# Optimization experiments

Measured on AMD Instinct MI355X. Metric: run time of the kernel, lower is better.

Reference implementation:

```python
import jax, jax.numpy as jnp
import numpy as np

N_HEADS = 12

def setup_inputs() -> dict:
    key = jax.random.key(0)
    ks = jax.random.split(key, 3)
    B, C, T = 4, 768, 2048
    x = jax.random.normal(ks[0], (B, C, T), dtype=jnp.float32)
    mask = jnp.ones((B, 1, 1, T), dtype=jnp.int32)  # all valid; masked_fill where mask==0
    Wqkv = jax.random.normal(ks[1], (3 * C, C), dtype=jnp.float32) * 0.02
    bqkv = jnp.zeros((3 * C,), dtype=jnp.float32)
    Wout = jax.random.normal(ks[2], (C, C), dtype=jnp.float32) * 0.02
    bout = jnp.zeros((C,), dtype=jnp.float32)
    return {"x": x, "mask": mask, "Wqkv": Wqkv, "bqkv": bqkv, "Wout": Wout, "bout": bout}


def reference(x, mask, Wqkv, bqkv, Wout, bout):
    B, C, T = x.shape
    H = N_HEADS
    d = C // H
    scale = 1.0 / jnp.sqrt(jnp.asarray(d, x.dtype))
    # 1x1 Conv1d == per-timestep matmul over channels
    qkv = jnp.einsum('oc,bct->bot', Wqkv, x) + bqkv[None, :, None]  # [B,3C,T]
    # channel dim splits as [3, H, d] per the torch view(B,3,H,d,T)
    qkv = qkv.reshape(B, 3, H, d, T).transpose(0, 1, 2, 4, 3)       # [B,3,H,T,d]
    q, k, v = qkv[:, 0], qkv[:, 1], qkv[:, 2]
    score = jnp.einsum('bhtd,bhsd->bhts', q, k) * scale             # [B,H,T,T]
    score = jnp.where(mask == 0, jnp.asarray(-10000.0, score.dtype), score)
    attn = jax.nn.softmax(score, axis=-1)  # dropout: eval mode (identity)
    o = jnp.einsum('bhts,bhsd->bhtd', attn, v)                      # [B,H,T,d]
    o = o.transpose(0, 1, 3, 2).reshape(B, C, T)                    # [B,C,T]
    return jnp.einsum('oc,bct->bot', Wout, o) + bout[None, :, None]
```

## Files before the change

### kernel.cpp

```cpp
#include <hip/hip_runtime.h>
#include <hip/hip_bf16.h>
#include <stdint.h>

#define B_   4
#define C_   768
#define T_   2048
#define H_   12
#define D_   64
#define O3_  2304

typedef __attribute__((ext_vector_type(4))) float f32x4;
typedef __attribute__((ext_vector_type(8))) short bf16x8;

__device__ __forceinline__ unsigned short f2bf(float f) {
  union { float f; unsigned int u; } v; v.f = f;
  unsigned int r = v.u + 0x7fffu + ((v.u >> 16) & 1u);
  return (unsigned short)(r >> 16);
}

__device__ __forceinline__ unsigned int pack2bf(float a, float b) {
  __hip_bfloat162 h2 = __float22bfloat162_rn(make_float2(a, b));
  union { __hip_bfloat162 h; unsigned int u; } cv; cv.h = h2;
  return cv.u;
}

__device__ __forceinline__ float fexp2(float x) {
#if __has_builtin(__builtin_amdgcn_exp2f)
  return __builtin_amdgcn_exp2f(x);
#else
  return exp2f(x);
#endif
}

__device__ __forceinline__ void async16(const void* g, void* lds) {
#if __has_builtin(__builtin_amdgcn_global_load_lds)
  __builtin_amdgcn_global_load_lds((const __attribute__((address_space(1))) void*)g,
                                   (__attribute__((address_space(3))) void*)lds, 16, 0, 0);
#else
  int lane = threadIdx.x & 63;
  *((uint4*)((char*)lds + lane * 16)) = *((const uint4*)g);
#endif
}


__global__ void cvt_f32_bf16(const float* __restrict__ in,
                             unsigned short* __restrict__ out, int n4) {
  int i = blockIdx.x * 256 + threadIdx.x;
  if (i < n4) {
    float4 f = ((const float4*)in)[i];
    ushort4 o;
    o.x = f2bf(f.x); o.y = f2bf(f.y); o.z = f2bf(f.z); o.w = f2bf(f.w);
    ((ushort4*)out)[i] = o;
  }
}

__global__ void make_bias(const int* __restrict__ mask, float* __restrict__ mbias, int n) {
  int i = blockIdx.x * 256 + threadIdx.x;
  if (i < n) mbias[i] = (mask[i] == 0) ? -14426.950408f : 0.0f;
}

__global__ void transpose_x(const float* __restrict__ x,
                            unsigned short* __restrict__ xT) {
  __shared__ unsigned short tile[32][33];
  int b = blockIdx.z;
  int c0 = blockIdx.y * 32;
  int t0 = blockIdx.x * 32;
  int tid = threadIdx.x;
  {
    int cl = tid >> 3;
    int tl = (tid & 7) * 4;
    float4 f = *(const float4*)(x + ((size_t)b * C_ + c0 + cl) * T_ + t0 + tl);
    tile[tl + 0][cl] = f2bf(f.x);
    tile[tl + 1][cl] = f2bf(f.y);
    tile[tl + 2][cl] = f2bf(f.z);
    tile[tl + 3][cl] = f2bf(f.w);
  }
  __syncthreads();
  {
    int tl = tid >> 3;
    int cl = (tid & 7) * 4;
    ushort4 o;
    o.x = tile[tl][cl + 0]; o.y = tile[tl][cl + 1];
    o.z = tile[tl][cl + 2]; o.w = tile[tl][cl + 3];
    *(ushort4*)(xT + ((size_t)b * T_ + t0 + tl) * C_ + c0 + cl) = o;
  }
}

__global__ __launch_bounds__(256)
void gemm_qkv(const unsigned short* __restrict__ xT,
              const unsigned short* __restrict__ W1,
              const float* __restrict__ bqkv,
              unsigned short* __restrict__ Qb,
              unsigned short* __restrict__ Kb,
              unsigned short* __restrict__ Vb) {
  __shared__ unsigned short sA[2][128 * 32];
  __shared__ unsigned short sB[2][128 * 32];

  const int b   = blockIdx.z;
  const int o0  = blockIdx.y * 128;
  const int t0  = blockIdx.x * 128;
  const int tid = threadIdx.x;
  const int wave = tid >> 6, lane = tid & 63;
  const int q = lane >> 4, ln = lane & 15;
  const int tw = wave >> 1, ow = wave & 1;

  const unsigned short* Ax = xT + (size_t)b * T_ * C_;
  const int srow = lane >> 2;
  const int scol = (lane & 3) * 8;

  const f32x4 ZERO = {0.f, 0.f, 0.f, 0.f};
  f32x4 acc[4][4];
#pragma unroll
  for (int mi = 0; mi < 4; ++mi)
#pragma unroll
    for (int ni = 0; ni < 4; ++ni) acc[mi][ni] = ZERO;

#pragma unroll
  for (int j = 0; j < 2; ++j) {
    const int chunk = wave * 2 + j;
    const int row = chunk * 16 + srow;
    async16(Ax + (size_t)(t0 + row) * C_ + scol, &sA[0][chunk * 512]);
    async16(W1 + (size_t)(o0 + row) * C_ + scol, &sB[0][chunk * 512]);
  }

  for (int i = 0; i < 24; ++i) {
    const int buf = i & 1;
    __syncthreads();
    if (i < 23) {
      const int k0 = (i + 1) * 32;
#pragma unroll
      for (int j = 0; j < 2; ++j) {
        const int chunk = wave * 2 + j;
        const int row = chunk * 16 + srow;
        async16(Ax + (size_t)(t0 + row) * C_ + k0 + scol, &sA[buf ^ 1][chunk * 512]);
        async16(W1 + (size_t)(o0 + row) * C_ + k0 + scol, &sB[buf ^ 1][chunk * 512]);
      }
    }

    bf16x8 aF[4], bF[4];
#pragma unroll
    for (int mi = 0; mi < 4; ++mi)
      aF[mi] = *(const bf16x8*)(&sA[buf][(tw * 64 + mi * 16 + ln) * 32 + q * 8]);
#pragma unroll
    for (int ni = 0; ni < 4; ++ni)
      bF[ni] = *(const bf16x8*)(&sB[buf][(ow * 64 + ni * 16 + ln) * 32 + q * 8]);
#pragma unroll
    for (int mi = 0; mi < 4; ++mi)
#pragma unroll
      for (int ni = 0; ni < 4; ++ni)
        acc[mi][ni] = __builtin_amdgcn_mfma_f32_16x16x32_bf16(aF[mi], bF[ni], acc[mi][ni], 0, 0, 0);
  }

  const float QSCL = 0.125f * 1.44269504f;
#pragma unroll
  for (int ni = 0; ni < 4; ++ni) {
    const int o = o0 + ow * 64 + ni * 16 + ln;
    const float bias = bqkv[o];
    const int which = o / C_;
    const int rem = o - which * C_;
    const int bh = b * H_ + (rem >> 6);
    const int dd = rem & 63;
#pragma unroll
    for (int mi = 0; mi < 4; ++mi) {
      const int tb = t0 + tw * 64 + mi * 16 + q * 4;
      f32x4 v = acc[mi][ni];
      if (which == 0) {
#pragma unroll
        for (int r = 0; r < 4; ++r)
          Qb[((size_t)bh * T_ + tb + r) * D_ + dd] = f2bf((v[r] + bias) * QSCL);
      } else if (which == 1) {
#pragma unroll
        for (int r = 0; r < 4; ++r) {
          const int s = tb + r;
          const int cp = (dd >> 3) ^ (s & 7);
          Kb[((size_t)bh * T_ + s) * 64 + (cp << 3) + (dd & 7)] = f2bf(v[r] + bias);
        }
      } else {
        const int tile = tb >> 6, si = tb & 63;
        const int cp = (si >> 3) ^ (dd & 7);
        ushort4 pk;
        pk.x = f2bf(v[0] + bias);
        pk.y = f2bf(v[1] + bias);
        pk.z = f2bf(v[2] + bias);
        pk.w = f2bf(v[3] + bias);
        *(ushort4*)(Vb + (((size_t)bh * 32 + tile) * 64 + dd) * 64 + (cp << 3) + (si & 7)) = pk;
      }
    }
  }
}

__global__ __launch_bounds__(256, 3)
void attn(const unsigned short* __restrict__ Qb,
          const unsigned short* __restrict__ Kb,
          const unsigned short* __restrict__ Vb,
          const float* __restrict__ mbias,
          unsigned short* __restrict__ Ob) {
  __shared__ __align__(16) char smem[32768];
  unsigned short* sK0 = (unsigned short*)smem;
  unsigned short* sV0 = (unsigned short*)(smem + 16384);

  const int id = blockIdx.x;
  const int bh = id % 48;
  const int tblk = id / 48;
  const int b = bh / H_, h = bh % H_;
  const int tid = threadIdx.x, wave = tid >> 6, lane = tid & 63;
  const int q = lane >> 4, ln = lane & 15;
  const int t0w = tblk * 128 + wave * 32;

  bf16x8 Qa[2][2];
#pragma unroll
  for (int tt = 0; tt < 2; ++tt) {
    const unsigned short* qrow = Qb + ((size_t)bh * T_ + t0w + tt * 16 + ln) * D_;
    Qa[tt][0] = *(const bf16x8*)(qrow + q * 8);
    Qa[tt][1] = *(const bf16x8*)(qrow + 32 + q * 8);
  }

  const f32x4 ZERO = {0.f, 0.f, 0.f, 0.f};
  f32x4 Oacc[4][2];
  f32x4 lacc[2];
#pragma unroll
  for (int dt = 0; dt < 4; ++dt)
#pragma unroll
    for (int tt = 0; tt < 2; ++tt) Oacc[dt][tt] = ZERO;
#pragma unroll
  for (int tt = 0; tt < 2; ++tt) lacc[tt] = ZERO;

  const short one_s = (ln == 0) ? (short)0x3F80 : (short)0;
  bf16x8 ones;
#pragma unroll
  for (int j = 0; j < 8; ++j) ones[j] = one_s;

  const unsigned short* gK = Kb + (size_t)bh * T_ * 64;
  const unsigned short* gV = Vb + (size_t)bh * 32 * 4096;

#pragma unroll
  for (int j = 0; j < 2; ++j) {
    const int chunk = wave * 2 + j;
    async16(gK + chunk * 512 + lane * 8, sK0 + chunk * 512);
    async16(gV + chunk * 512 + lane * 8, sV0 + chunk * 512);
  }

  for (int it = 0; it < 32; ++it) {
    const int buf = it & 1;
    __syncthreads();
    if (it < 31) {
      const unsigned short* k = gK + (it + 1) * 4096;
      const unsigned short* v = gV + (it + 1) * 4096;
      unsigned short* dK = sK0 + (buf ^ 1) * 4096;
      unsigned short* dV = sV0 + (buf ^ 1) * 4096;
#pragma unroll
      for (int j = 0; j < 2; ++j) {
        const int chunk = wave * 2 + j;
        async16(k + chunk * 512 + lane * 8, dK + chunk * 512);
        async16(v + chunk * 512 + lane * 8, dV + chunk * 512);
      }
    }

    const int s0 = it * 64;
    const float bvl = mbias[b * T_ + s0 + lane];
    const bool anymask = (__ballot(bvl != 0.0f) != 0ull);
    const unsigned short* sKc = sK0 + buf * 4096;
    const unsigned short* sVc = sV0 + buf * 4096;

    bf16x8 pf[2][2];
#pragma unroll
    for (int kc = 0; kc < 2; ++kc) {
      bf16x8 kf[2][2];
#pragma unroll
      for (int sb = 0; sb < 2; ++sb) {
        const unsigned short* krow = sKc + (kc * 32 + sb * 16 + ln) * 64;
        kf[sb][0] = *(const bf16x8*)(krow + ((q ^ (ln & 7)) << 3));
        kf[sb][1] = *(const bf16x8*)(krow + (((4 + q) ^ (ln & 7)) << 3));
      }
#pragma unroll
      for (int tt = 0; tt < 2; ++tt) {
        f32x4 sc[2];
#pragma unroll
        for (int sb = 0; sb < 2; ++sb) {
          f32x4 p0 = __builtin_amdgcn_mfma_f32_16x16x32_bf16(kf[sb][0], Qa[tt][0], ZERO, 0, 0, 0);
          sc[sb]   = __builtin_amdgcn_mfma_f32_16x16x32_bf16(kf[sb][1], Qa[tt][1], p0, 0, 0, 0);
          if (anymask) {
            f32x4 bb = *(const f32x4*)(mbias + b * T_ + s0 + kc * 32 + sb * 16 + q * 4);
#pragma unroll
            for (int r = 0; r < 4; ++r) sc[sb][r] += bb[r];
          }
        }
        unsigned int A0 = pack2bf(fexp2(sc[0][0]), fexp2(sc[0][1]));
        unsigned int B0 = pack2bf(fexp2(sc[0][2]), fexp2(sc[0][3]));
        unsigned int C0 = pack2bf(fexp2(sc[1][0]), fexp2(sc[1][1]));
        unsigned int E0 = pack2bf(fexp2(sc[1][2]), fexp2(sc[1][3]));
        asm volatile("v_permlane32_swap_b32 %0, %1" : "+v"(A0), "+v"(C0));
        asm volatile("v_permlane16_swap_b32 %0, %1" : "+v"(A0), "+v"(C0));
        asm volatile("v_permlane32_swap_b32 %0, %1" : "+v"(B0), "+v"(E0));
        asm volatile("v_permlane16_swap_b32 %0, %1" : "+v"(B0), "+v"(E0));
        union { bf16x8 v; unsigned int u[4]; } P;
        P.u[0] = A0;
        P.u[1] = B0;
        P.u[2] = C0;
        P.u[3] = E0;
        pf[tt][kc] = P.v;
      }
    }

#pragma unroll
    for (int dt = 0; dt < 4; ++dt) {
#pragma unroll
      for (int kc = 0; kc < 2; ++kc) {
        bf16x8 vf = *(const bf16x8*)(sVc + (dt * 16 + ln) * 64 +
                                     (((kc * 4 + q) ^ (ln & 7)) << 3));
#pragma unroll
        for (int tt = 0; tt < 2; ++tt)
          Oacc[dt][tt] = __builtin_amdgcn_mfma_f32_16x16x32_bf16(vf, pf[tt][kc], Oacc[dt][tt], 0, 0, 0);
      }
    }
#pragma unroll
    for (int kc = 0; kc < 2; ++kc)
#pragma unroll
      for (int tt = 0; tt < 2; ++tt)
        lacc[tt] = __builtin_amdgcn_mfma_f32_16x16x32_bf16(ones, pf[tt][kc], lacc[tt], 0, 0, 0);
  }

#pragma unroll
  for (int tt = 0; tt < 2; ++tt) {
    const float lv = __shfl(lacc[tt][0], ln, 64);
    const float inv = 1.0f / lv;
    const int t = t0w + tt * 16 + ln;
#pragma unroll
    for (int dt = 0; dt < 4; ++dt) {
      f32x4 o = Oacc[dt][tt];
      ushort4 pk;
      pk.x = f2bf(o[0] * inv);
      pk.y = f2bf(o[1] * inv);
      pk.z = f2bf(o[2] * inv);
      pk.w = f2bf(o[3] * inv);
      *(ushort4*)(Ob + ((size_t)b * T_ + t) * C_ + h * D_ + dt * 16 + q * 4) = pk;
    }
  }
}

__global__ __launch_bounds__(256)
void gemm_out(const unsigned short* __restrict__ Ob,
              const unsigned short* __restrict__ W2,
              const float* __restrict__ bout,
              float* __restrict__ out) {
  __shared__ unsigned short sA[2][128 * 32];
  __shared__ unsigned short sB[2][128 * 32];

  const int b   = blockIdx.z;
  const int o0  = blockIdx.y * 128;
  const int t0  = blockIdx.x * 128;
  const int tid = threadIdx.x;
  const int wave = tid >> 6, lane = tid & 63;
  const int q = lane >> 4, ln = lane & 15;
  const int tw = wave >> 1, ow = wave & 1;

  const unsigned short* Bo = Ob + (size_t)b * T_ * C_;
  const int srow = lane >> 2;
  const int scol = (lane & 3) * 8;

  const f32x4 ZERO = {0.f, 0.f, 0.f, 0.f};
  f32x4 acc[4][4];
#pragma unroll
  for (int mi = 0; mi < 4; ++mi)
#pragma unroll
    for (int ni = 0; ni < 4; ++ni) acc[mi][ni] = ZERO;

#pragma unroll
  for (int j = 0; j < 2; ++j) {
    const int chunk = wave * 2 + j;
    const int row = chunk * 16 + srow;
    async16(W2 + (size_t)(o0 + row) * C_ + scol, &sA[0][chunk * 512]);
    async16(Bo + (size_t)(t0 + row) * C_ + scol, &sB[0][chunk * 512]);
  }

  for (int i = 0; i < 24; ++i) {
    const int buf = i & 1;
    __syncthreads();
    if (i < 23) {
      const int k0 = (i + 1) * 32;
#pragma unroll
      for (int j = 0; j < 2; ++j) {
        const int chunk = wave * 2 + j;
        const int row = chunk * 16 + srow;
        async16(W2 + (size_t)(o0 + row) * C_ + k0 + scol, &sA[buf ^ 1][chunk * 512]);
        async16(Bo + (size_t)(t0 + row) * C_ + k0 + scol, &sB[buf ^ 1][chunk * 512]);
      }
    }

    bf16x8 aF[4], bF[4];
#pragma unroll
    for (int mi = 0; mi < 4; ++mi)
      aF[mi] = *(const bf16x8*)(&sA[buf][(tw * 64 + mi * 16 + ln) * 32 + q * 8]);
#pragma unroll
    for (int ni = 0; ni < 4; ++ni)
      bF[ni] = *(const bf16x8*)(&sB[buf][(ow * 64 + ni * 16 + ln) * 32 + q * 8]);
#pragma unroll
    for (int mi = 0; mi < 4; ++mi)
#pragma unroll
      for (int ni = 0; ni < 4; ++ni)
        acc[mi][ni] = __builtin_amdgcn_mfma_f32_16x16x32_bf16(aF[mi], bF[ni], acc[mi][ni], 0, 0, 0);
  }

#pragma unroll
  for (int mi = 0; mi < 4; ++mi) {
    const int ob = o0 + tw * 64 + mi * 16 + q * 4;
#pragma unroll
    for (int ni = 0; ni < 4; ++ni) {
      const int t = t0 + ow * 64 + ni * 16 + ln;
      f32x4 v = acc[mi][ni];
#pragma unroll
      for (int r = 0; r < 4; ++r)
        out[((size_t)b * C_ + ob + r) * T_ + t] = v[r] + bout[ob + r];
    }
  }
}


extern "C" void kernel_launch(void* const* d_in, const int* in_sizes, int n_in,
                              void* d_out, int out_size, void* d_ws, size_t ws_size,
                              hipStream_t stream) {
  (void)in_sizes; (void)n_in; (void)out_size; (void)ws_size;
  const float* x    = (const float*)d_in[0];
  const int*   mask = (const int*)d_in[1];
  const float* Wqkv = (const float*)d_in[2];
  const float* bqkv = (const float*)d_in[3];
  const float* Wout = (const float*)d_in[4];
  const float* bout = (const float*)d_in[5];
  float* out = (float*)d_out;

  const size_t szHead = (size_t)B_ * H_ * T_ * D_;
  const size_t szBTC  = (size_t)B_ * T_ * C_;
  unsigned short* Qb  = (unsigned short*)d_ws;
  unsigned short* Kb  = Qb + szHead;
  unsigned short* Vb  = Kb + szHead;
  unsigned short* Ob  = Vb + szHead;
  unsigned short* xT  = Ob + szBTC;
  unsigned short* W1b = xT + szBTC;
  unsigned short* W2b = W1b + (size_t)O3_ * C_;
  float* mbias        = (float*)(W2b + (size_t)C_ * C_);

  cvt_f32_bf16<<<dim3((O3_ * C_ / 4 + 255) / 256), 256, 0, stream>>>(Wqkv, W1b, O3_ * C_ / 4);
  cvt_f32_bf16<<<dim3((C_ * C_ / 4 + 255) / 256), 256, 0, stream>>>(Wout, W2b, C_ * C_ / 4);
  make_bias<<<dim3((B_ * T_ + 255) / 256), 256, 0, stream>>>(mask, mbias, B_ * T_);
  transpose_x<<<dim3(T_ / 32, C_ / 32, B_), 256, 0, stream>>>(x, xT);
  gemm_qkv<<<dim3(T_ / 128, O3_ / 128, B_), 256, 0, stream>>>(xT, W1b, bqkv, Qb, Kb, Vb);
  attn<<<dim3(768), 256, 0, stream>>>(Qb, Kb, Vb, mbias, Ob);
  gemm_out<<<dim3(T_ / 128, C_ / 128, B_), 256, 0, stream>>>(Ob, W2b, bout, out);
}
```

Before: 228.4 us.

## Software-pipeline attention loop: overlap QK of next tile with PV of current

```diff
diff --git a/kernel.cpp b/kernel.cpp
--- a/kernel.cpp
+++ b/kernel.cpp
@@ -232,55 +232,37 @@
 
   const unsigned short* gK = Kb + (size_t)bh * T_ * 64;
   const unsigned short* gV = Vb + (size_t)bh * 32 * 4096;
-
-#pragma unroll
-  for (int j = 0; j < 2; ++j) {
-    const int chunk = wave * 2 + j;
-    async16(gK + chunk * 512 + lane * 8, sK0 + chunk * 512);
-    async16(gV + chunk * 512 + lane * 8, sV0 + chunk * 512);
-  }
-
-  for (int it = 0; it < 32; ++it) {
-    const int buf = it & 1;
-    __syncthreads();
-    if (it < 31) {
-      const unsigned short* k = gK + (it + 1) * 4096;
-      const unsigned short* v = gV + (it + 1) * 4096;
-      unsigned short* dK = sK0 + (buf ^ 1) * 4096;
-      unsigned short* dV = sV0 + (buf ^ 1) * 4096;
-#pragma unroll
-      for (int j = 0; j < 2; ++j) {
-        const int chunk = wave * 2 + j;
-        async16(k + chunk * 512 + lane * 8, dK + chunk * 512);
-        async16(v + chunk * 512 + lane * 8, dV + chunk * 512);
-      }
-    }
-
-    const int s0 = it * 64;
-    const float bvl = mbias[b * T_ + s0 + lane];
+  const float* mb = mbias + b * T_;
+
+  auto stage4 = [&](const unsigned short* g, unsigned short* lds) {
+#pragma unroll
+    for (int j = 0; j < 2; ++j) {
+      const int chunk = wave * 2 + j;
+      async16(g + chunk * 512 + lane * 8, lds + chunk * 512);
+    }
+  };
+
+  auto QK = [&](const unsigned short* sKc, int s0, bf16x8 pfO[2][2]) {
+    const float bvl = mb[s0 + lane];
     const bool anymask = (__ballot(bvl != 0.0f) != 0ull);
-    const unsigned short* sKc = sK0 + buf * 4096;
-    const unsigned short* sVc = sV0 + buf * 4096;
-
-    bf16x8 pf[2][2];
 #pragma unroll
     for (int kc = 0; kc < 2; ++kc) {
-      bf16x8 kf[2][2];
+      bf16x8 kf0[2], kf1[2];
 #pragma unroll
       for (int sb = 0; sb < 2; ++sb) {
         const unsigned short* krow = sKc + (kc * 32 + sb * 16 + ln) * 64;
-        kf[sb][0] = *(const bf16x8*)(krow + ((q ^ (ln & 7)) << 3));
-        kf[sb][1] = *(const bf16x8*)(krow + (((4 + q) ^ (ln & 7)) << 3));
+        kf0[sb] = *(const bf16x8*)(krow + ((q ^ (ln & 7)) << 3));
+        kf1[sb] = *(const bf16x8*)(krow + (((4 + q) ^ (ln & 7)) << 3));
       }
 #pragma unroll
       for (int tt = 0; tt < 2; ++tt) {
         f32x4 sc[2];
 #pragma unroll
         for (int sb = 0; sb < 2; ++sb) {
-          f32x4 p0 = __builtin_amdgcn_mfma_f32_16x16x32_bf16(kf[sb][0], Qa[tt][0], ZERO, 0, 0, 0);
-          sc[sb]   = __builtin_amdgcn_mfma_f32_16x16x32_bf16(kf[sb][1], Qa[tt][1], p0, 0, 0, 0);
+          f32x4 p0 = __builtin_amdgcn_mfma_f32_16x16x32_bf16(kf0[sb], Qa[tt][0], ZERO, 0, 0, 0);
+          sc[sb]   = __builtin_amdgcn_mfma_f32_16x16x32_bf16(kf1[sb], Qa[tt][1], p0, 0, 0, 0);
           if (anymask) {
-            f32x4 bb = *(const f32x4*)(mbias + b * T_ + s0 + kc * 32 + sb * 16 + q * 4);
+            f32x4 bb = *(const f32x4*)(mb + s0 + kc * 32 + sb * 16 + q * 4);
 #pragma unroll
             for (int r = 0; r < 4; ++r) sc[sb][r] += bb[r];
           }
@@ -298,10 +280,12 @@
         P.u[1] = B0;
         P.u[2] = C0;
         P.u[3] = E0;
-        pf[tt][kc] = P.v;
-      }
-    }
-
+        pfO[tt][kc] = P.v;
+      }
+    }
+  };
+
+  auto PV = [&](const unsigned short* sVc, bf16x8 pfI[2][2]) {
 #pragma unroll
     for (int dt = 0; dt < 4; ++dt) {
 #pragma unroll
@@ -310,15 +294,44 @@
                                      (((kc * 4 + q) ^ (ln & 7)) << 3));
 #pragma unroll
         for (int tt = 0; tt < 2; ++tt)
-          Oacc[dt][tt] = __builtin_amdgcn_mfma_f32_16x16x32_bf16(vf, pf[tt][kc], Oacc[dt][tt], 0, 0, 0);
+          Oacc[dt][tt] = __builtin_amdgcn_mfma_f32_16x16x32_bf16(vf, pfI[tt][kc], Oacc[dt][tt], 0, 0, 0);
       }
     }
 #pragma unroll
     for (int kc = 0; kc < 2; ++kc)
 #pragma unroll
       for (int tt = 0; tt < 2; ++tt)
-        lacc[tt] = __builtin_amdgcn_mfma_f32_16x16x32_bf16(ones, pf[tt][kc], lacc[tt], 0, 0, 0);
-  }
+        lacc[tt] = __builtin_amdgcn_mfma_f32_16x16x32_bf16(ones, pfI[tt][kc], lacc[tt], 0, 0, 0);
+  };
+
+  bf16x8 pfA[2][2], pfB[2][2];
+
+  stage4(gK, sK0);
+  stage4(gV, sV0);
+  __syncthreads();
+  stage4(gK + 4096, sK0 + 4096);
+  QK(sK0, 0, pfA);
+
+  for (int ith = 0; ith < 15; ++ith) {
+    const int it = ith * 2;
+    __syncthreads();
+    stage4(gK + (size_t)(it + 2) * 4096, sK0);
+    stage4(gV + (size_t)(it + 1) * 4096, sV0 + 4096);
+    QK(sK0 + 4096, (it + 1) * 64, pfB);
+    PV(sV0, pfA);
+    __syncthreads();
+    stage4(gK + (size_t)(it + 3) * 4096, sK0 + 4096);
+    stage4(gV + (size_t)(it + 2) * 4096, sV0);
+    QK(sK0, (it + 2) * 64, pfA);
+    PV(sV0 + 4096, pfB);
+  }
+
+  __syncthreads();
+  stage4(gV + (size_t)31 * 4096, sV0 + 4096);
+  QK(sK0 + 4096, 31 * 64, pfB);
+  PV(sV0, pfA);
+  __syncthreads();
+  PV(sV0 + 4096, pfB);
 
 #pragma unroll
   for (int tt = 0; tt < 2; ++tt) {
```

Result: no change. 228.4 us (+0.0%).
